# Kernel tuning notes

Measured on AMD Instinct MI355X. Metric: run time of the kernel, lower is better.

The kernel has to match this reference:

```python
import jax, jax.numpy as jnp
import numpy as np

N_NODES = 100000
N_EDGES = 1600000
IN_C, HID_C, OUT_C = 128, 128, 64


def setup_inputs() -> dict:
    key = jax.random.key(0)
    ks = jax.random.split(key, 5)
    x = jax.random.normal(ks[0], (N_NODES, IN_C), dtype=jnp.float32)
    edge_index = jax.random.randint(ks[1], (2, N_EDGES), 0, N_NODES, dtype=jnp.int32)
    W1 = jax.random.normal(ks[2], (IN_C, HID_C), dtype=jnp.float32) * (1.0 / np.sqrt(IN_C))
    W2 = jax.random.normal(ks[3], (HID_C, HID_C), dtype=jnp.float32) * (1.0 / np.sqrt(HID_C))
    W3 = jax.random.normal(ks[4], (HID_C, OUT_C), dtype=jnp.float32) * (1.0 / np.sqrt(HID_C))
    b1 = jnp.zeros((HID_C,), jnp.float32)
    b2 = jnp.zeros((HID_C,), jnp.float32)
    b3 = jnp.zeros((OUT_C,), jnp.float32)
    return {"x": x, "edge_index": edge_index, "W1": W1, "b1": b1,
            "W2": W2, "b2": b2, "W3": W3, "b3": b3}


def _gcn_norm(edge_index, num_nodes):
    # PyG gcn_norm: add self-loops, symmetric normalization D^-1/2 A D^-1/2
    loops = jnp.arange(num_nodes, dtype=edge_index.dtype)
    row = jnp.concatenate([edge_index[0], loops])  # source nodes
    col = jnp.concatenate([edge_index[1], loops])  # target nodes
    ones = jnp.ones(row.shape[0], jnp.float32)
    deg = jax.ops.segment_sum(ones, col, num_segments=num_nodes)
    dinv = jnp.where(deg > 0, jax.lax.rsqrt(deg), 0.0)
    norm = dinv[row] * dinv[col]  # [E + N]
    return row, col, norm


def _gcn_conv(h, row, col, norm, W, b, num_nodes):
    h = h @ W                                   # [N, out] dense transform first
    msg = h[row] * norm[:, None]                # gather + scale, [E+N, out]
    out = jax.ops.segment_sum(msg, col, num_segments=num_nodes)  # scatter-add
    return out + b


def reference(x, edge_index, W1, b1, W2, b2, W3, b3):
    n = x.shape[0]
    row, col, norm = _gcn_norm(edge_index, n)
    h = jax.nn.relu(_gcn_conv(x, row, col, norm, W1, b1, n))
    h = jax.nn.relu(_gcn_conv(h, row, col, norm, W2, b2, n))
    h = _gcn_conv(h, row, col, norm, W3, b3, n)
    return h
```

## Files before the change

kernel.cpp:

```cpp
#include <hip/hip_runtime.h>
#include <hip/hip_fp16.h>


#define K_DIM 128
#define CHUNK 8192
#define NBMAX 1024
#define BSH 8
#define BMASK 255

typedef _Float16 f16x8 __attribute__((ext_vector_type(8)));
typedef float f32x4 __attribute__((ext_vector_type(4)));


__global__ __launch_bounds__(256) void hist_pass(const int* __restrict__ col, int E,
                                                 int NB, int B1, int* __restrict__ histG) {
    __shared__ int h[NBMAX];
    const int tid = threadIdx.x;
    for (int i = tid; i < NB; i += 256) h[i] = 0;
    __syncthreads();
    const int base = blockIdx.x * CHUNK;
    const int end = min(base + CHUNK, E);
    for (int e = base + tid; e < end; e += 256) atomicAdd(&h[col[e] >> BSH], 1);
    __syncthreads();
    for (int i = tid; i < NB; i += 256) histG[(size_t)i * B1 + blockIdx.x] = h[i];
}

__global__ __launch_bounds__(256) void scan_blocks(int* __restrict__ data, int n,
                                                   int* __restrict__ bsum) {
    __shared__ int sh[256];
    const int tid = threadIdx.x;
    const int base = blockIdx.x * 1024;
    int v[4];
    int sum = 0;
#pragma unroll
    for (int j = 0; j < 4; ++j) {
        int i = base + tid * 4 + j;
        v[j] = (i < n) ? data[i] : 0;
        sum += v[j];
    }
    sh[tid] = sum;
    __syncthreads();
#pragma unroll
    for (int off = 1; off < 256; off <<= 1) {
        int t = (tid >= off) ? sh[tid - off] : 0;
        __syncthreads();
        sh[tid] += t;
        __syncthreads();
    }
    int run = (tid > 0) ? sh[tid - 1] : 0;
#pragma unroll
    for (int j = 0; j < 4; ++j) {
        int i = base + tid * 4 + j;
        if (i < n) data[i] = run;
        run += v[j];
    }
    if (tid == 255) bsum[blockIdx.x] = sh[255];
}

__global__ __launch_bounds__(256) void scan_single(int* __restrict__ data, int n) {
    __shared__ int sh[256];
    const int tid = threadIdx.x;
    int v[4];
    int sum = 0;
#pragma unroll
    for (int j = 0; j < 4; ++j) {
        int i = tid * 4 + j;
        v[j] = (i < n) ? data[i] : 0;
        sum += v[j];
    }
    sh[tid] = sum;
    __syncthreads();
#pragma unroll
    for (int off = 1; off < 256; off <<= 1) {
        int t = (tid >= off) ? sh[tid - off] : 0;
        __syncthreads();
        sh[tid] += t;
        __syncthreads();
    }
    int run = (tid > 0) ? sh[tid - 1] : 0;
#pragma unroll
    for (int j = 0; j < 4; ++j) {
        int i = tid * 4 + j;
        if (i < n) data[i] = run;
        run += v[j];
    }
}

__global__ __launch_bounds__(256) void scatter_pass(const int* __restrict__ row,
                                                    const int* __restrict__ col, int E,
                                                    int NB, int B1,
                                                    const int* __restrict__ histG,
                                                    const int* __restrict__ bsum,
                                                    int* __restrict__ ebuf) {
    __shared__ int cur[NBMAX];
    const int tid = threadIdx.x;
    for (int i = tid; i < NB; i += 256) {
        const size_t idx = (size_t)i * B1 + blockIdx.x;
        cur[i] = histG[idx] + bsum[idx >> 10];
    }
    __syncthreads();
    const int base = blockIdx.x * CHUNK;
    const int end = min(base + CHUNK, E);
    for (int e = base + tid; e < end; e += 256) {
        int d = col[e];
        int s = row[e];
        int pos = atomicAdd(&cur[d >> BSH], 1);
        ebuf[pos] = (s << BSH) | (d & BMASK);
    }
}

__global__ __launch_bounds__(256) void build_csr(const int* __restrict__ ebuf,
                                                 const int* __restrict__ histG,
                                                 const int* __restrict__ bsum,
                                                 int NB, int B1, int N, int E,
                                                 int* __restrict__ offs,
                                                 float* __restrict__ dinv,
                                                 int* __restrict__ csr) {
    __shared__ int cnt[256];
    __shared__ int scn[256];
    __shared__ int curL[256];
    const int tid = threadIdx.x;
    const int b = blockIdx.x;
    const size_t iS = (size_t)b * B1;
    const int S = histG[iS] + bsum[iS >> 10];
    int T = E;
    if (b + 1 < NB) {
        const size_t iT = (size_t)(b + 1) * B1;
        T = histG[iT] + bsum[iT >> 10];
    }

    cnt[tid] = 0;
    __syncthreads();
    for (int i = S + tid; i < T; i += 256) atomicAdd(&cnt[ebuf[i] & BMASK], 1);
    __syncthreads();
    scn[tid] = cnt[tid];
    __syncthreads();
#pragma unroll
    for (int off = 1; off < 256; off <<= 1) {
        int t = (tid >= off) ? scn[tid - off] : 0;
        __syncthreads();
        scn[tid] += t;
        __syncthreads();
    }
    {
        int exc = (tid > 0) ? scn[tid - 1] : 0;
        int node = b * 256 + tid;
        if (node < N) {
            offs[node] = S + exc;
            dinv[node] = rsqrtf((float)(cnt[tid] + 1));
        }
        curL[tid] = S + exc;
    }
    if (b == 0 && tid == 0) offs[N] = E;
    __syncthreads();
    for (int i = S + tid; i < T; i += 256) {
        int p = ebuf[i];
        int pos = atomicAdd(&curL[p & BMASK], 1);
        csr[pos] = p >> BSH;
    }
}

__global__ void prep_wT(const float* __restrict__ W1, const float* __restrict__ W2,
                        const float* __restrict__ W3, __half* __restrict__ wT1,
                        __half* __restrict__ wT2, __half* __restrict__ wT3) {
    int tid = blockIdx.x * 256 + threadIdx.x;
    if (tid < 16384) {
        int n = tid >> 7, k = tid & 127;
        wT1[tid] = __float2half(W1[k * 128 + n]);
    } else if (tid < 32768) {
        int t = tid - 16384;
        int n = t >> 7, k = t & 127;
        wT2[t] = __float2half(W2[k * 128 + n]);
    } else if (tid < 40960) {
        int t = tid - 32768;
        int n = t >> 7, k = t & 127;
        wT3[t] = __float2half(W3[k * 64 + n]);
    }
}


__global__ __launch_bounds__(256) void gemm_x(const float* __restrict__ X,
                                              const __half* __restrict__ wT,
                                              const float* __restrict__ dinv,
                                              __half* __restrict__ out, int M) {
    const int tid = threadIdx.x;
    const int wave = tid >> 6;
    const int l = tid & 63;
    const int lm = l & 15;
    const int kg = l >> 4;
    const int row0 = blockIdx.x * 128 + wave * 32;

    f32x4 acc[2][8];
#pragma unroll
    for (int mt = 0; mt < 2; ++mt)
#pragma unroll
        for (int nt = 0; nt < 8; ++nt) acc[mt][nt] = {0.f, 0.f, 0.f, 0.f};

    const int m0 = row0 + lm;
    const int m1 = row0 + 16 + lm;
    const int mc0 = min(m0, M - 1);
    const int mc1 = min(m1, M - 1);

#pragma unroll
    for (int ks = 0; ks < 4; ++ks) {
        const int k0 = ks * 32 + kg * 8;
        float4 u0 = *(const float4*)&X[(size_t)mc0 * 128 + k0];
        float4 u1 = *(const float4*)&X[(size_t)mc0 * 128 + k0 + 4];
        float4 u2 = *(const float4*)&X[(size_t)mc1 * 128 + k0];
        float4 u3 = *(const float4*)&X[(size_t)mc1 * 128 + k0 + 4];
        f16x8 b0 = {(_Float16)u0.x, (_Float16)u0.y, (_Float16)u0.z, (_Float16)u0.w,
                    (_Float16)u1.x, (_Float16)u1.y, (_Float16)u1.z, (_Float16)u1.w};
        f16x8 b1 = {(_Float16)u2.x, (_Float16)u2.y, (_Float16)u2.z, (_Float16)u2.w,
                    (_Float16)u3.x, (_Float16)u3.y, (_Float16)u3.z, (_Float16)u3.w};
#pragma unroll
        for (int nt = 0; nt < 8; ++nt) {
            f16x8 a = *(const f16x8*)&wT[(size_t)(nt * 16 + lm) * 128 + k0];
            acc[0][nt] = __builtin_amdgcn_mfma_f32_16x16x32_f16(a, b0, acc[0][nt], 0, 0, 0);
            acc[1][nt] = __builtin_amdgcn_mfma_f32_16x16x32_f16(a, b1, acc[1][nt], 0, 0, 0);
        }
    }

#pragma unroll
    for (int mt = 0; mt < 2; ++mt) {
        const int m = (mt == 0) ? m0 : m1;
        if (m < M) {
            const float dv = dinv[m];
#pragma unroll
            for (int nt = 0; nt < 8; ++nt) {
                float z0 = acc[mt][nt][0] * dv, z1 = acc[mt][nt][1] * dv;
                float z2 = acc[mt][nt][2] * dv, z3 = acc[mt][nt][3] * dv;
                __half2 o[2] = {__float22half2_rn(make_float2(z0, z1)),
                                __float22half2_rn(make_float2(z2, z3))};
                *(float2*)&out[(size_t)m * 128 + nt * 16 + kg * 4] = *(float2*)o;
            }
        }
    }
}


template <int NCOLS>
__global__ __launch_bounds__(256) void gemm_f16(const __half* __restrict__ A,
                                                const __half* __restrict__ wT,
                                                const float* __restrict__ dinv,
                                                __half* __restrict__ out, int M) {
    constexpr int NT = NCOLS / 16;
    __shared__ __half sWT[NCOLS][136];

    const int tid = threadIdx.x;
    for (int idx = tid; idx < NCOLS * 16; idx += 256) {
        int n = idx >> 4, kc = (idx & 15) * 8;
        *(float4*)&sWT[n][kc] = *(const float4*)&wT[n * 128 + kc];
    }
    __syncthreads();

    const int wave = tid >> 6;
    const int l = tid & 63;
    const int lm = l & 15;
    const int kg = l >> 4;
    const int row0 = blockIdx.x * 128 + wave * 32;

    f32x4 acc[2][NT];
#pragma unroll
    for (int mt = 0; mt < 2; ++mt)
#pragma unroll
        for (int nt = 0; nt < NT; ++nt) acc[mt][nt] = {0.f, 0.f, 0.f, 0.f};

    const int m0 = row0 + lm;
    const int m1 = row0 + 16 + lm;
    const int mc0 = min(m0, M - 1);
    const int mc1 = min(m1, M - 1);

#pragma unroll
    for (int ks = 0; ks < 4; ++ks) {
        const int k0 = ks * 32 + kg * 8;
        f16x8 b0 = *(const f16x8*)&A[(size_t)mc0 * 128 + k0];
        f16x8 b1 = *(const f16x8*)&A[(size_t)mc1 * 128 + k0];
#pragma unroll
        for (int nt = 0; nt < NT; ++nt) {
            f16x8 a = *(const f16x8*)&sWT[nt * 16 + lm][k0];
            acc[0][nt] = __builtin_amdgcn_mfma_f32_16x16x32_f16(a, b0, acc[0][nt], 0, 0, 0);
            acc[1][nt] = __builtin_amdgcn_mfma_f32_16x16x32_f16(a, b1, acc[1][nt], 0, 0, 0);
        }
    }

#pragma unroll
    for (int mt = 0; mt < 2; ++mt) {
        const int m = (mt == 0) ? m0 : m1;
        if (m < M) {
            const float dv = dinv[m];
#pragma unroll
            for (int nt = 0; nt < NT; ++nt) {
                float z0 = acc[mt][nt][0] * dv, z1 = acc[mt][nt][1] * dv;
                float z2 = acc[mt][nt][2] * dv, z3 = acc[mt][nt][3] * dv;
                __half2 o[2] = {__float22half2_rn(make_float2(z0, z1)),
                                __float22half2_rn(make_float2(z2, z3))};
                *(float2*)&out[(size_t)m * NCOLS + nt * 16 + kg * 4] = *(float2*)o;
            }
        }
    }
}


template <bool RELU>
__global__ __launch_bounds__(256) void agg128(const __half* __restrict__ h,
                                              const float* __restrict__ dinv,
                                              const int* __restrict__ offs,
                                              const int* __restrict__ csr,
                                              const float* __restrict__ bias,
                                              __half* __restrict__ out, int N) {
    const int wid = (blockIdx.x * 256 + threadIdx.x) >> 6;
    if (wid >= N) return;
    const int l = threadIdx.x & 63;
    const int q = l >> 4;
    const int c = l & 15;
    const int beg = offs[wid], end = offs[wid + 1];
    const float di = dinv[wid];
    const float4* __restrict__ hp = (const float4*)h;

    float a[8] = {0.f, 0.f, 0.f, 0.f, 0.f, 0.f, 0.f, 0.f};
    int e = beg;
    for (; e + 16 <= end; e += 16) {
        int s0 = csr[e + q];
        int s1 = csr[e + 4 + q];
        int s2 = csr[e + 8 + q];
        int s3 = csr[e + 12 + q];
        float4 r0 = hp[(size_t)s0 * 16 + c];
        float4 r1 = hp[(size_t)s1 * 16 + c];
        float4 r2 = hp[(size_t)s2 * 16 + c];
        float4 r3 = hp[(size_t)s3 * 16 + c];
        const __half* h0 = (const __half*)&r0;
        const __half* h1 = (const __half*)&r1;
        const __half* h2 = (const __half*)&r2;
        const __half* h3 = (const __half*)&r3;
#pragma unroll
        for (int j = 0; j < 8; ++j) a[j] += __half2float(h0[j]);
#pragma unroll
        for (int j = 0; j < 8; ++j) a[j] += __half2float(h1[j]);
#pragma unroll
        for (int j = 0; j < 8; ++j) a[j] += __half2float(h2[j]);
#pragma unroll
        for (int j = 0; j < 8; ++j) a[j] += __half2float(h3[j]);
    }
    for (; e < end; e += 8) {
        const int last = end - 1;
        int i0 = e + q, i1 = e + 4 + q;
        float m0 = (i0 < end) ? 1.f : 0.f;
        float m1 = (i1 < end) ? 1.f : 0.f;
        int s0 = csr[min(i0, last)];
        int s1 = csr[min(i1, last)];
        float4 r0 = hp[(size_t)s0 * 16 + c];
        float4 r1 = hp[(size_t)s1 * 16 + c];
        const __half* h0 = (const __half*)&r0;
        const __half* h1 = (const __half*)&r1;
#pragma unroll
        for (int j = 0; j < 8; ++j) a[j] = fmaf(__half2float(h0[j]), m0, a[j]);
#pragma unroll
        for (int j = 0; j < 8; ++j) a[j] = fmaf(__half2float(h1[j]), m1, a[j]);
    }
#pragma unroll
    for (int j = 0; j < 8; ++j) {
        a[j] += __shfl_xor(a[j], 16);
        a[j] += __shfl_xor(a[j], 32);
    }
    {
        float4 rs = hp[(size_t)wid * 16 + c];
        const __half* hs = (const __half*)&rs;
#pragma unroll
        for (int j = 0; j < 8; ++j) a[j] += __half2float(hs[j]);
    }
    float4 b0 = ((const float4*)bias)[2 * c];
    float4 b1 = ((const float4*)bias)[2 * c + 1];
    float z[8];
    z[0] = fmaf(di, a[0], b0.x); z[1] = fmaf(di, a[1], b0.y);
    z[2] = fmaf(di, a[2], b0.z); z[3] = fmaf(di, a[3], b0.w);
    z[4] = fmaf(di, a[4], b1.x); z[5] = fmaf(di, a[5], b1.y);
    z[6] = fmaf(di, a[6], b1.z); z[7] = fmaf(di, a[7], b1.w);
    if (RELU) {
#pragma unroll
        for (int j = 0; j < 8; ++j) z[j] = fmaxf(z[j], 0.f);
    }
    if (q == 0) {
        __half2 o[4] = {__float22half2_rn(make_float2(z[0], z[1])),
                        __float22half2_rn(make_float2(z[2], z[3])),
                        __float22half2_rn(make_float2(z[4], z[5])),
                        __float22half2_rn(make_float2(z[6], z[7]))};
        ((float4*)out)[(size_t)wid * 16 + c] = *(float4*)o;
    }
}

__global__ __launch_bounds__(256) void agg64(const __half* __restrict__ h,
                                             const float* __restrict__ dinv,
                                             const int* __restrict__ offs,
                                             const int* __restrict__ csr,
                                             const float* __restrict__ bias,
                                             float* __restrict__ out, int N) {
    const int wid = (blockIdx.x * 256 + threadIdx.x) >> 6;
    if (wid >= N) return;
    const int l = threadIdx.x & 63;
    const int q = l >> 3;
    const int c = l & 7;
    const int beg = offs[wid], end = offs[wid + 1];
    const float di = dinv[wid];
    const float4* __restrict__ hp = (const float4*)h;

    float a[8] = {0.f, 0.f, 0.f, 0.f, 0.f, 0.f, 0.f, 0.f};
    int e = beg;
    for (; e + 16 <= end; e += 16) {
        int s0 = csr[e + q];
        int s1 = csr[e + 8 + q];
        float4 r0 = hp[(size_t)s0 * 8 + c];
        float4 r1 = hp[(size_t)s1 * 8 + c];
        const __half* h0 = (const __half*)&r0;
        const __half* h1 = (const __half*)&r1;
#pragma unroll
        for (int j = 0; j < 8; ++j) a[j] += __half2float(h0[j]);
#pragma unroll
        for (int j = 0; j < 8; ++j) a[j] += __half2float(h1[j]);
    }
    for (; e < end; e += 8) {
        const int last = end - 1;
        int i0 = e + q;
        float m0 = (i0 < end) ? 1.f : 0.f;
        int s0 = csr[min(i0, last)];
        float4 r0 = hp[(size_t)s0 * 8 + c];
        const __half* h0 = (const __half*)&r0;
#pragma unroll
        for (int j = 0; j < 8; ++j) a[j] = fmaf(__half2float(h0[j]), m0, a[j]);
    }
#pragma unroll
    for (int j = 0; j < 8; ++j) {
        a[j] += __shfl_xor(a[j], 8);
        a[j] += __shfl_xor(a[j], 16);
        a[j] += __shfl_xor(a[j], 32);
    }
    {
        float4 rs = hp[(size_t)wid * 8 + c];
        const __half* hs = (const __half*)&rs;
#pragma unroll
        for (int j = 0; j < 8; ++j) a[j] += __half2float(hs[j]);
    }
    float4 b0 = ((const float4*)bias)[2 * c];
    float4 b1 = ((const float4*)bias)[2 * c + 1];
    float z[8];
    z[0] = fmaf(di, a[0], b0.x); z[1] = fmaf(di, a[1], b0.y);
    z[2] = fmaf(di, a[2], b0.z); z[3] = fmaf(di, a[3], b0.w);
    z[4] = fmaf(di, a[4], b1.x); z[5] = fmaf(di, a[5], b1.y);
    z[6] = fmaf(di, a[6], b1.z); z[7] = fmaf(di, a[7], b1.w);
    if (q == 0) {
        ((float4*)out)[(size_t)wid * 16 + 2 * c] = make_float4(z[0], z[1], z[2], z[3]);
        ((float4*)out)[(size_t)wid * 16 + 2 * c + 1] = make_float4(z[4], z[5], z[6], z[7]);
    }
}


extern "C" void kernel_launch(void* const* d_in, const int* in_sizes, int n_in,
                              void* d_out, int out_size, void* d_ws, size_t ws_size,
                              hipStream_t stream) {
    const float* x  = (const float*)d_in[0];
    const int*   ei = (const int*)d_in[1];
    const float* W1 = (const float*)d_in[2];
    const float* b1 = (const float*)d_in[3];
    const float* W2 = (const float*)d_in[4];
    const float* b2 = (const float*)d_in[5];
    const float* W3 = (const float*)d_in[6];
    const float* b3 = (const float*)d_in[7];

    const int N = in_sizes[0] / 128;
    const int E = in_sizes[1] / 2;
    const int* row = ei;
    const int* col = ei + E;

    const int NB = (N + BMASK) >> BSH;
    const int B1 = (E + CHUNK - 1) / CHUNK;
    const int NBB1 = NB * B1;

    char* p = (char*)d_ws;
    auto alloc = [&](size_t bytes) {
        char* r = p;
        p += (bytes + 255) & ~(size_t)255;
        return r;
    };
    int*    offs  = (int*)alloc((size_t)(N + 1) * 4);
    float*  dinv  = (float*)alloc((size_t)N * 4);
    int*    histG = (int*)alloc((size_t)NBB1 * 4);
    int*    bsum  = (int*)alloc(1024 * 4);
    int*    ebuf  = (int*)alloc((size_t)E * 4);
    int*    csr   = (int*)alloc((size_t)E * 4);
    __half* bufA  = (__half*)alloc((size_t)N * 128 * 2);
    __half* bufB  = (__half*)alloc((size_t)N * 128 * 2);
    __half* wT1   = (__half*)alloc(16384 * 2);
    __half* wT2   = (__half*)alloc(16384 * 2);
    __half* wT3   = (__half*)alloc(8192 * 2);

    const int nsb = (NBB1 + 1023) / 1024;

    hist_pass<<<B1, 256, 0, stream>>>(col, E, NB, B1, histG);
    scan_blocks<<<nsb, 256, 0, stream>>>(histG, NBB1, bsum);
    scan_single<<<1, 256, 0, stream>>>(bsum, nsb);
    scatter_pass<<<B1, 256, 0, stream>>>(row, col, E, NB, B1, histG, bsum, ebuf);
    build_csr<<<NB, 256, 0, stream>>>(ebuf, histG, bsum, NB, B1, N, E, offs, dinv, csr);

    prep_wT<<<160, 256, 0, stream>>>(W1, W2, W3, wT1, wT2, wT3);

    const int gTile = (N + 127) / 128;
    const int gAgg = (N + 3) / 4;

    gemm_x<<<gTile, 256, 0, stream>>>(x, wT1, dinv, bufA, N);
    agg128<true><<<gAgg, 256, 0, stream>>>(bufA, dinv, offs, csr, b1, bufB, N);

    gemm_f16<128><<<gTile, 256, 0, stream>>>(bufB, wT2, dinv, bufA, N);
    agg128<true><<<gAgg, 256, 0, stream>>>(bufA, dinv, offs, csr, b2, bufB, N);

    gemm_f16<64><<<gTile, 256, 0, stream>>>(bufB, wT3, dinv, bufA, N);
    agg64<<<gAgg, 256, 0, stream>>>(bufA, dinv, offs, csr, b3, (float*)d_out, N);
}
```

Baseline: 280.0 us.

## Split aggregation into two column-half passes and vectorize histogram/scatter loads

After: 360.0 us. 28.6% more time.

```diff
diff --git a/kernel.cpp b/kernel.cpp
--- a/kernel.cpp
+++ b/kernel.cpp
@@ -3,7 +3,7 @@
 
 
 #define K_DIM 128
-#define CHUNK 8192
+#define CHUNK 4096
 #define NBMAX 1024
 #define BSH 8
 #define BMASK 255
@@ -19,8 +19,19 @@
     for (int i = tid; i < NB; i += 256) h[i] = 0;
     __syncthreads();
     const int base = blockIdx.x * CHUNK;
-    const int end = min(base + CHUNK, E);
-    for (int e = base + tid; e < end; e += 256) atomicAdd(&h[col[e] >> BSH], 1);
+    const int bend = min(base + CHUNK, E);
+    for (int idx = base + tid * 4; idx < bend; idx += 1024) {
+        if (idx + 4 <= bend) {
+            int4 c4 = *(const int4*)&col[idx];
+            atomicAdd(&h[c4.x >> BSH], 1);
+            atomicAdd(&h[c4.y >> BSH], 1);
+            atomicAdd(&h[c4.z >> BSH], 1);
+            atomicAdd(&h[c4.w >> BSH], 1);
+        } else {
+            for (int j = 0; j < 4 && idx + j < bend; ++j)
+                atomicAdd(&h[col[idx + j] >> BSH], 1);
+        }
+    }
     __syncthreads();
     for (int i = tid; i < NB; i += 256) histG[(size_t)i * B1 + blockIdx.x] = h[i];
 }
@@ -100,12 +111,27 @@
     }
     __syncthreads();
     const int base = blockIdx.x * CHUNK;
-    const int end = min(base + CHUNK, E);
-    for (int e = base + tid; e < end; e += 256) {
-        int d = col[e];
-        int s = row[e];
-        int pos = atomicAdd(&cur[d >> BSH], 1);
-        ebuf[pos] = (s << BSH) | (d & BMASK);
+    const int bend = min(base + CHUNK, E);
+    for (int idx = base + tid * 4; idx < bend; idx += 1024) {
+        if (idx + 4 <= bend) {
+            int4 d4 = *(const int4*)&col[idx];
+            int4 s4 = *(const int4*)&row[idx];
+            int p0 = atomicAdd(&cur[d4.x >> BSH], 1);
+            ebuf[p0] = (s4.x << BSH) | (d4.x & BMASK);
+            int p1 = atomicAdd(&cur[d4.y >> BSH], 1);
+            ebuf[p1] = (s4.y << BSH) | (d4.y & BMASK);
+            int p2 = atomicAdd(&cur[d4.z >> BSH], 1);
+            ebuf[p2] = (s4.z << BSH) | (d4.z & BMASK);
+            int p3 = atomicAdd(&cur[d4.w >> BSH], 1);
+            ebuf[p3] = (s4.w << BSH) | (d4.w & BMASK);
+        } else {
+            for (int j = 0; j < 4 && idx + j < bend; ++j) {
+                int d = col[idx + j];
+                int s = row[idx + j];
+                int pos = atomicAdd(&cur[d >> BSH], 1);
+                ebuf[pos] = (s << BSH) | (d & BMASK);
+            }
+        }
     }
 }
 
@@ -302,17 +328,17 @@
 
 
 template <bool RELU>
-__global__ __launch_bounds__(256) void agg128(const __half* __restrict__ h,
-                                              const float* __restrict__ dinv,
-                                              const int* __restrict__ offs,
-                                              const int* __restrict__ csr,
-                                              const float* __restrict__ bias,
-                                              __half* __restrict__ out, int N) {
+__global__ __launch_bounds__(256) void agg128h(const __half* __restrict__ h,
+                                               const float* __restrict__ dinv,
+                                               const int* __restrict__ offs,
+                                               const int* __restrict__ csr,
+                                               const float* __restrict__ bias,
+                                               __half* __restrict__ out, int N, int half) {
     const int wid = (blockIdx.x * 256 + threadIdx.x) >> 6;
     if (wid >= N) return;
     const int l = threadIdx.x & 63;
-    const int q = l >> 4;
-    const int c = l & 15;
+    const int q = l >> 3;
+    const int cc = half * 8 + (l & 7);
     const int beg = offs[wid], end = offs[wid + 1];
     const float di = dinv[wid];
     const float4* __restrict__ hp = (const float4*)h;
@@ -321,55 +347,40 @@
     int e = beg;
     for (; e + 16 <= end; e += 16) {
         int s0 = csr[e + q];
-        int s1 = csr[e + 4 + q];
-        int s2 = csr[e + 8 + q];
-        int s3 = csr[e + 12 + q];
-        float4 r0 = hp[(size_t)s0 * 16 + c];
-        float4 r1 = hp[(size_t)s1 * 16 + c];
-        float4 r2 = hp[(size_t)s2 * 16 + c];
-        float4 r3 = hp[(size_t)s3 * 16 + c];
+        int s1 = csr[e + 8 + q];
+        float4 r0 = hp[(size_t)s0 * 16 + cc];
+        float4 r1 = hp[(size_t)s1 * 16 + cc];
         const __half* h0 = (const __half*)&r0;
         const __half* h1 = (const __half*)&r1;
-        const __half* h2 = (const __half*)&r2;
-        const __half* h3 = (const __half*)&r3;
 #pragma unroll
         for (int j = 0; j < 8; ++j) a[j] += __half2float(h0[j]);
 #pragma unroll
         for (int j = 0; j < 8; ++j) a[j] += __half2float(h1[j]);
-#pragma unroll
-        for (int j = 0; j < 8; ++j) a[j] += __half2float(h2[j]);
-#pragma unroll
-        for (int j = 0; j < 8; ++j) a[j] += __half2float(h3[j]);
     }
     for (; e < end; e += 8) {
         const int last = end - 1;
-        int i0 = e + q, i1 = e + 4 + q;
+        int i0 = e + q;
         float m0 = (i0 < end) ? 1.f : 0.f;
-        float m1 = (i1 < end) ? 1.f : 0.f;
         int s0 = csr[min(i0, last)];
-        int s1 = csr[min(i1, last)];
-        float4 r0 = hp[(size_t)s0 * 16 + c];
-        float4 r1 = hp[(size_t)s1 * 16 + c];
+        float4 r0 = hp[(size_t)s0 * 16 + cc];
         const __half* h0 = (const __half*)&r0;
-        const __half* h1 = (const __half*)&r1;
 #pragma unroll
         for (int j = 0; j < 8; ++j) a[j] = fmaf(__half2float(h0[j]), m0, a[j]);
-#pragma unroll
-        for (int j = 0; j < 8; ++j) a[j] = fmaf(__half2float(h1[j]), m1, a[j]);
     }
 #pragma unroll
     for (int j = 0; j < 8; ++j) {
+        a[j] += __shfl_xor(a[j], 8);
         a[j] += __shfl_xor(a[j], 16);
         a[j] += __shfl_xor(a[j], 32);
     }
     {
-        float4 rs = hp[(size_t)wid * 16 + c];
+        float4 rs = hp[(size_t)wid * 16 + cc];
         const __half* hs = (const __half*)&rs;
 #pragma unroll
         for (int j = 0; j < 8; ++j) a[j] += __half2float(hs[j]);
     }
-    float4 b0 = ((const float4*)bias)[2 * c];
-    float4 b1 = ((const float4*)bias)[2 * c + 1];
+    float4 b0 = ((const float4*)bias)[2 * cc];
+    float4 b1 = ((const float4*)bias)[2 * cc + 1];
     float z[8];
     z[0] = fmaf(di, a[0], b0.x); z[1] = fmaf(di, a[1], b0.y);
     z[2] = fmaf(di, a[2], b0.z); z[3] = fmaf(di, a[3], b0.w);
@@ -384,32 +395,32 @@
                         __float22half2_rn(make_float2(z[2], z[3])),
                         __float22half2_rn(make_float2(z[4], z[5])),
                         __float22half2_rn(make_float2(z[6], z[7]))};
-        ((float4*)out)[(size_t)wid * 16 + c] = *(float4*)o;
-    }
-}
-
-__global__ __launch_bounds__(256) void agg64(const __half* __restrict__ h,
-                                             const float* __restrict__ dinv,
-                                             const int* __restrict__ offs,
-                                             const int* __restrict__ csr,
-                                             const float* __restrict__ bias,
-                                             float* __restrict__ out, int N) {
+        ((float4*)out)[(size_t)wid * 16 + cc] = *(float4*)o;
+    }
+}
+
+__global__ __launch_bounds__(256) void agg64h(const __half* __restrict__ h,
+                                              const float* __restrict__ dinv,
+                                              const int* __restrict__ offs,
+                                              const int* __restrict__ csr,
+                                              const float* __restrict__ bias,
+                                              float* __restrict__ out, int N, int half) {
     const int wid = (blockIdx.x * 256 + threadIdx.x) >> 6;
     if (wid >= N) return;
     const int l = threadIdx.x & 63;
-    const int q = l >> 3;
-    const int c = l & 7;
+    const int q = l >> 2;
+    const int cc = half * 4 + (l & 3);
     const int beg = offs[wid], end = offs[wid + 1];
     const float di = dinv[wid];
     const float4* __restrict__ hp = (const float4*)h;
 
     float a[8] = {0.f, 0.f, 0.f, 0.f, 0.f, 0.f, 0.f, 0.f};
     int e = beg;
-    for (; e + 16 <= end; e += 16) {
+    for (; e + 32 <= end; e += 32) {
         int s0 = csr[e + q];
-        int s1 = csr[e + 8 + q];
-        float4 r0 = hp[(size_t)s0 * 8 + c];
-        float4 r1 = hp[(size_t)s1 * 8 + c];
+        int s1 = csr[e + 16 + q];
+        float4 r0 = hp[(size_t)s0 * 8 + cc];
+        float4 r1 = hp[(size_t)s1 * 8 + cc];
         const __half* h0 = (const __half*)&r0;
         const __half* h1 = (const __half*)&r1;
 #pragma unroll
@@ -417,38 +428,39 @@
 #pragma unroll
         for (int j = 0; j < 8; ++j) a[j] += __half2float(h1[j]);
     }
-    for (; e < end; e += 8) {
+    for (; e < end; e += 16) {
         const int last = end - 1;
         int i0 = e + q;
         float m0 = (i0 < end) ? 1.f : 0.f;
         int s0 = csr[min(i0, last)];
-        float4 r0 = hp[(size_t)s0 * 8 + c];
+        float4 r0 = hp[(size_t)s0 * 8 + cc];
         const __half* h0 = (const __half*)&r0;
 #pragma unroll
         for (int j = 0; j < 8; ++j) a[j] = fmaf(__half2float(h0[j]), m0, a[j]);
     }
 #pragma unroll
     for (int j = 0; j < 8; ++j) {
+        a[j] += __shfl_xor(a[j], 4);
         a[j] += __shfl_xor(a[j], 8);
         a[j] += __shfl_xor(a[j], 16);
         a[j] += __shfl_xor(a[j], 32);
     }
     {
-        float4 rs = hp[(size_t)wid * 8 + c];
+        float4 rs = hp[(size_t)wid * 8 + cc];
         const __half* hs = (const __half*)&rs;
 #pragma unroll
         for (int j = 0; j < 8; ++j) a[j] += __half2float(hs[j]);
     }
-    float4 b0 = ((const float4*)bias)[2 * c];
-    float4 b1 = ((const float4*)bias)[2 * c + 1];
+    float4 b0 = ((const float4*)bias)[2 * cc];
+    float4 b1 = ((const float4*)bias)[2 * cc + 1];
     float z[8];
     z[0] = fmaf(di, a[0], b0.x); z[1] = fmaf(di, a[1], b0.y);
     z[2] = fmaf(di, a[2], b0.z); z[3] = fmaf(di, a[3], b0.w);
     z[4] = fmaf(di, a[4], b1.x); z[5] = fmaf(di, a[5], b1.y);
     z[6] = fmaf(di, a[6], b1.z); z[7] = fmaf(di, a[7], b1.w);
     if (q == 0) {
-        ((float4*)out)[(size_t)wid * 16 + 2 * c] = make_float4(z[0], z[1], z[2], z[3]);
-        ((float4*)out)[(size_t)wid * 16 + 2 * c + 1] = make_float4(z[4], z[5], z[6], z[7]);
+        ((float4*)out)[(size_t)wid * 16 + 2 * cc] = make_float4(z[0], z[1], z[2], z[3]);
+        ((float4*)out)[(size_t)wid * 16 + 2 * cc + 1] = make_float4(z[4], z[5], z[6], z[7]);
     }
 }
 
@@ -506,11 +518,14 @@
     const int gAgg = (N + 3) / 4;
 
     gemm_x<<<gTile, 256, 0, stream>>>(x, wT1, dinv, bufA, N);
-    agg128<true><<<gAgg, 256, 0, stream>>>(bufA, dinv, offs, csr, b1, bufB, N);
+    agg128h<true><<<gAgg, 256, 0, stream>>>(bufA, dinv, offs, csr, b1, bufB, N, 0);
+    agg128h<true><<<gAgg, 256, 0, stream>>>(bufA, dinv, offs, csr, b1, bufB, N, 1);
 
     gemm_f16<128><<<gTile, 256, 0, stream>>>(bufB, wT2, dinv, bufA, N);
-    agg128<true><<<gAgg, 256, 0, stream>>>(bufA, dinv, offs, csr, b2, bufB, N);
+    agg128h<true><<<gAgg, 256, 0, stream>>>(bufA, dinv, offs, csr, b2, bufB, N, 0);
+    agg128h<true><<<gAgg, 256, 0, stream>>>(bufA, dinv, offs, csr, b2, bufB, N, 1);
 
     gemm_f16<64><<<gTile, 256, 0, stream>>>(bufB, wT3, dinv, bufA, N);
-    agg64<<<gAgg, 256, 0, stream>>>(bufA, dinv, offs, csr, b3, (float*)d_out, N);
-}
+    agg64h<<<gAgg, 256, 0, stream>>>(bufA, dinv, offs, csr, b3, (float*)d_out, N, 0);
+    agg64h<<<gAgg, 256, 0, stream>>>(bufA, dinv, offs, csr, b3, (float*)d_out, N, 1);
+}
```
